# Performance work log

Hardware: AMD Instinct MI355X
Metric: run time of the kernel (lower is better)

Reference implementation:

```python
import jax, jax.numpy as jnp
import numpy as np
import itertools

DIM, ORDER = 8, 4  # matches init_kwargs

def _exponent_table(dim, order):
    # All multisets (non-decreasing tuples) of size 0..order over range(dim),
    # sorted lexicographically -- identical to sorted(Counter keys) in the torch code
    # (Counter keys are sorted tuples; combinations_with_replacement yields exactly those).
    terms = sorted(itertools.chain.from_iterable(
        itertools.combinations_with_replacement(range(dim), o) for o in range(order + 1)))
    E = np.zeros((len(terms), dim), dtype=np.int32)
    for i, t in enumerate(terms):
        for d in t:
            E[i, d] += 1
    return E

E = jnp.asarray(_exponent_table(DIM, ORDER))  # [nterms=495, dim=8]


def setup_inputs() -> dict:
    key = jax.random.key(0)
    x = jax.random.normal(key, (65536, DIM), dtype=jnp.float32)
    return {"x": x}


def reference(x):
    # torch: cat_i prod_d x[..., d] ** ind_i.count(d)
    # vectorized: broadcast pow with exponent table, reduce-product over dim axis
    # x: [B, dim] -> [B, 1, dim] ** [nterms, dim] -> prod over dim -> [B, nterms]
    return jnp.prod(x[..., None, :] ** E, axis=-1)
```

## Files before the change

### kernel.cpp

```cpp
#include <hip/hip_runtime.h>


struct Specs {
    unsigned short uv[64][8];
    unsigned short pp[64];
};

constexpr int pidx_c(int a, int b) {
    return 9 + 8 * a - (a * (a - 1)) / 2 + (b - a);
}

constexpr Specs make_specs() {
    Specs S{};
    for (int l = 0; l < 64; ++l) {
        int s1 = 0, s2 = 0, u1 = 0, u2 = 0;
        if (l >= 1 && l <= 8) { s1 = l - 1; u1 = 1; }
        else if (l >= 9 && l < 45) {
            int k = l - 9, i = 0;
            while (k >= 8 - i) { k -= 8 - i; ++i; }
            s1 = i; s2 = i + k; u1 = 1; u2 = 1;
        }
        S.pp[l] = (unsigned short)(s1 | (s2 << 4) | (u1 << 8) | (u2 << 9));
    }
    int idx = 1;
    for (int a = 0; a < 8; ++a) {
        S.uv[idx & 63][idx >> 6] = (unsigned short)(1 + a); ++idx;
        for (int b = a; b < 8; ++b) {
            S.uv[idx & 63][idx >> 6] = (unsigned short)pidx_c(a, b); ++idx;
            for (int c = b; c < 8; ++c) {
                S.uv[idx & 63][idx >> 6] =
                    (unsigned short)(pidx_c(a, b) | ((1 + c) << 8)); ++idx;
                for (int d = c; d < 8; ++d) {
                    S.uv[idx & 63][idx >> 6] =
                        (unsigned short)(pidx_c(a, b) | (pidx_c(c, d) << 8));
                    ++idx;
                }
            }
        }
    }
    return S;
}

__constant__ Specs SPECS = make_specs();

#define WAVES_PER_BLOCK 4
#define ROWS_PER_WAVE   8
#define ROWS_PER_BLOCK  (WAVES_PER_BLOCK * ROWS_PER_WAVE)

__global__ __launch_bounds__(256, 8) void TotalDegree_29755533426739_kernel(
    const float* __restrict__ x, float* __restrict__ out, int B) {
    __shared__ float xs[ROWS_PER_BLOCK * 8];

    const int tid  = (int)threadIdx.x;
    const int lane = tid & 63;
    const int wid  = tid >> 6;

    {
        const int gi = (int)blockIdx.x * (ROWS_PER_BLOCK * 8) + tid;
        xs[tid] = (gi < B * 8) ? x[gi] : 0.0f;
    }

    const int ppv  = (int)SPECS.pp[lane];
    const int s1   = ppv & 15;
    const int s2   = (ppv >> 4) & 15;
    const bool use1 = ((ppv >> 8) & 1) != 0;
    const bool use2 = ((ppv >> 9) & 1) != 0;

    int u4[8], v4[8];
    #pragma unroll
    for (int c = 0; c < 8; ++c) {
        const int sp = (int)SPECS.uv[lane][c];
        u4[c] = (sp & 255) << 2;
        v4[c] = (sp >> 8) << 2;
    }

    __syncthreads();

    const float* xw = xs + wid * (ROWS_PER_WAVE * 8);
    const unsigned baseRow =
        (unsigned)blockIdx.x * ROWS_PER_BLOCK + (unsigned)(wid * ROWS_PER_WAVE);
    unsigned off = baseRow * 495u + (unsigned)lane;

    #pragma unroll 2
    for (int rr = 0; rr < ROWS_PER_WAVE; ++rr) {
        const float a1 = xw[rr * 8 + s1];
        const float a2 = xw[rr * 8 + s2];
        const float P  = (use1 ? a1 : 1.0f) * (use2 ? a2 : 1.0f);
        const int  Pi  = __float_as_int(P);

        #pragma unroll
        for (int c = 0; c < 8; ++c) {
            const float f1 = __int_as_float(__builtin_amdgcn_ds_bpermute(u4[c], Pi));
            const float f2 = __int_as_float(__builtin_amdgcn_ds_bpermute(v4[c], Pi));
            const float tv = f1 * f2;
            if (c < 7) {
                out[off + (unsigned)(c * 64)] = tv;
            } else if (lane < 47) {
                out[off + 448u] = tv;
            }
        }
        off += 495u;
    }
}

extern "C" void kernel_launch(void* const* d_in, const int* in_sizes, int n_in,
                              void* d_out, int out_size, void* d_ws, size_t ws_size,
                              hipStream_t stream) {
    const float* x = (const float*)d_in[0];
    float* out = (float*)d_out;
    const int B = in_sizes[0] / 8;
    const int grid = (B + ROWS_PER_BLOCK - 1) / ROWS_PER_BLOCK;
    hipLaunchKernelGGL(TotalDegree_29755533426739_kernel,
                       dim3(grid), dim3(256), 0, stream, x, out, B);
}
```

Before: 129.9 us.

## Group four rows per chunk to emit 16-byte vectorized output stores

Processes four output rows (1980 floats, 16-byte aligned) as one contiguous chunk, so each lane writes float4 stores instead of scalar dword stores. A repacked constant table holds per-lane permute indices for four elements at a time. Chunks that straddle two rows do extra bpermutes and a select. The aim is fewer store instructions and wider global writes, at the cost of more cross-lane permutes and more register pressure.

```diff
diff --git a/kernel.cpp b/kernel.cpp
--- a/kernel.cpp
+++ b/kernel.cpp
@@ -2,7 +2,7 @@
 
 
 struct Specs {
-    unsigned short uv[64][8];
+    unsigned kspec[8][64][2];
     unsigned short pp[64];
 };
 
@@ -22,22 +22,36 @@
         }
         S.pp[l] = (unsigned short)(s1 | (s2 << 4) | (u1 << 8) | (u2 << 9));
     }
+    unsigned short uv[495] = {};
     int idx = 1;
     for (int a = 0; a < 8; ++a) {
-        S.uv[idx & 63][idx >> 6] = (unsigned short)(1 + a); ++idx;
+        uv[idx++] = (unsigned short)(1 + a);
         for (int b = a; b < 8; ++b) {
-            S.uv[idx & 63][idx >> 6] = (unsigned short)pidx_c(a, b); ++idx;
+            uv[idx++] = (unsigned short)pidx_c(a, b);
             for (int c = b; c < 8; ++c) {
-                S.uv[idx & 63][idx >> 6] =
-                    (unsigned short)(pidx_c(a, b) | ((1 + c) << 8)); ++idx;
-                for (int d = c; d < 8; ++d) {
-                    S.uv[idx & 63][idx >> 6] =
-                        (unsigned short)(pidx_c(a, b) | (pidx_c(c, d) << 8));
-                    ++idx;
-                }
+                uv[idx++] = (unsigned short)(pidx_c(a, b) | ((1 + c) << 8));
+                for (int d = c; d < 8; ++d)
+                    uv[idx++] = (unsigned short)(pidx_c(a, b) | (pidx_c(c, d) << 8));
             }
         }
     }
+    for (int k = 0; k < 8; ++k)
+        for (int l = 0; l < 64; ++l) {
+            unsigned w0 = 0, w1 = 0;
+            for (int s = 0; s < 4; ++s) {
+                int e = k * 256 + l * 4 + s;
+                unsigned field = 0;
+                if (e < 1980) {
+                    int t = e % 495;
+                    unsigned u = uv[t] & 255u, v = uv[t] >> 8;
+                    field = (u << 2) | ((v << 2) << 8);
+                }
+                if (s < 2) w0 |= field << (s * 16);
+                else       w1 |= field << ((s - 2) * 16);
+            }
+            S.kspec[k][l][0] = w0;
+            S.kspec[k][l][1] = w1;
+        }
     return S;
 }
 
@@ -66,40 +80,67 @@
     const bool use1 = ((ppv >> 8) & 1) != 0;
     const bool use2 = ((ppv >> 9) & 1) != 0;
 
-    int u4[8], v4[8];
+    unsigned kw0[8], kw1[8];
     #pragma unroll
-    for (int c = 0; c < 8; ++c) {
-        const int sp = (int)SPECS.uv[lane][c];
-        u4[c] = (sp & 255) << 2;
-        v4[c] = (sp >> 8) << 2;
+    for (int k = 0; k < 8; ++k) {
+        kw0[k] = SPECS.kspec[k][lane][0];
+        kw1[k] = SPECS.kspec[k][lane][1];
     }
 
     __syncthreads();
 
+    constexpr int RA[8]  = {0, 0, 1, 1, 2, 2, 3, 3};
+    constexpr int RB[8]  = {0, 1, 1, 2, 2, 3, 3, 3};
+    constexpr int THR[8] = {0, 239, 0, 222, 0, 205, 0, 0};
+
     const float* xw = xs + wid * (ROWS_PER_WAVE * 8);
-    const unsigned baseRow =
-        (unsigned)blockIdx.x * ROWS_PER_BLOCK + (unsigned)(wid * ROWS_PER_WAVE);
-    unsigned off = baseRow * 495u + (unsigned)lane;
+    const unsigned grp0 =
+        ((unsigned)blockIdx.x * ROWS_PER_BLOCK + (unsigned)(wid * ROWS_PER_WAVE)) >> 2;
 
-    #pragma unroll 2
-    for (int rr = 0; rr < ROWS_PER_WAVE; ++rr) {
-        const float a1 = xw[rr * 8 + s1];
-        const float a2 = xw[rr * 8 + s2];
-        const float P  = (use1 ? a1 : 1.0f) * (use2 ? a2 : 1.0f);
-        const int  Pi  = __float_as_int(P);
+    #pragma unroll
+    for (int gg = 0; gg < ROWS_PER_WAVE / 4; ++gg) {
+        const unsigned grp = grp0 + (unsigned)gg;
+        if ((int)(grp * 4) >= B) break;
+
+        float Pr[4];
+        #pragma unroll
+        for (int r = 0; r < 4; ++r) {
+            const int xb = (gg * 4 + r) * 8;
+            const float a1 = xw[xb + s1];
+            const float a2 = xw[xb + s2];
+            Pr[r] = (use1 ? a1 : 1.0f) * (use2 ? a2 : 1.0f);
+        }
+
+        float* gbase = out + (size_t)grp * 1980u;
 
         #pragma unroll
-        for (int c = 0; c < 8; ++c) {
-            const float f1 = __int_as_float(__builtin_amdgcn_ds_bpermute(u4[c], Pi));
-            const float f2 = __int_as_float(__builtin_amdgcn_ds_bpermute(v4[c], Pi));
-            const float tv = f1 * f2;
-            if (c < 7) {
-                out[off + (unsigned)(c * 64)] = tv;
+        for (int k = 0; k < 8; ++k) {
+            const int PaI = __float_as_int(Pr[RA[k]]);
+            const int PbI = __float_as_int(Pr[RB[k]]);
+            float4 val;
+            #pragma unroll
+            for (int s = 0; s < 4; ++s) {
+                const unsigned w = (s < 2) ? kw0[k] : kw1[k];
+                const unsigned field = (s & 1) ? (w >> 16) : (w & 0xffffu);
+                const int u4 = (int)(field & 0xffu);
+                const int v4 = (int)((field >> 8) & 0xffu);
+                float f1 = __int_as_float(__builtin_amdgcn_ds_bpermute(u4, PaI));
+                float f2 = __int_as_float(__builtin_amdgcn_ds_bpermute(v4, PaI));
+                if (RA[k] != RB[k]) {
+                    const float g1 = __int_as_float(__builtin_amdgcn_ds_bpermute(u4, PbI));
+                    const float g2 = __int_as_float(__builtin_amdgcn_ds_bpermute(v4, PbI));
+                    const bool useA = lane < ((THR[k] - s + 3) >> 2);
+                    f1 = useA ? f1 : g1;
+                    f2 = useA ? f2 : g2;
+                }
+                (&val.x)[s] = f1 * f2;
+            }
+            if (k < 7) {
+                *(float4*)(gbase + k * 256 + lane * 4) = val;
             } else if (lane < 47) {
-                out[off + 448u] = tv;
+                *(float4*)(gbase + 1792 + lane * 4) = val;
             }
         }
-        off += 495u;
     }
 }
 
```

Result: slower. 145.8 us (+12.2%).
